# Optimization experiments

Measured on AMD Instinct MI355X. Metric: run time of the kernel, lower is better.

## Reference

```python
import jax, jax.numpy as jnp
import numpy as np

NUM_HEADS = 16
D_MODEL = 1024
D_K = D_MODEL // NUM_HEADS


def setup_inputs() -> dict:
    key = jax.random.key(0)
    ks = jax.random.split(key, 6)
    B, S = 4, 2048
    x = jax.random.normal(ks[0], (B, S, D_MODEL), dtype=jnp.float32)
    scale = 1.0 / np.sqrt(D_MODEL)
    W_q = jax.random.normal(ks[1], (D_MODEL, D_MODEL), dtype=jnp.float32) * scale
    W_k = jax.random.normal(ks[2], (D_MODEL, D_MODEL), dtype=jnp.float32) * scale
    W_v = jax.random.normal(ks[3], (D_MODEL, D_MODEL), dtype=jnp.float32) * scale
    W_o = jax.random.normal(ks[4], (D_MODEL, D_MODEL), dtype=jnp.float32) * scale
    b_o = jnp.zeros((D_MODEL,), dtype=jnp.float32)
    return {"x": x, "W_q": W_q, "W_k": W_k, "W_v": W_v, "W_o": W_o, "b_o": b_o}


def reference(x, W_q, W_k, W_v, W_o, b_o):
    B, S, D = x.shape
    H, dk = NUM_HEADS, D_K
    # torch nn.Linear computes x @ W.T
    q = (x @ W_q.T).reshape(B, S, H, dk).transpose(0, 2, 1, 3)  # [B,H,S,dk]
    k = (x @ W_k.T).reshape(B, S, H, dk).transpose(0, 2, 1, 3)
    v = (x @ W_v.T).reshape(B, S, H, dk).transpose(0, 2, 1, 3)
    scores = jnp.einsum('bhqd,bhkd->bhqk', q, k) / jnp.sqrt(jnp.float32(dk))
    causal = jnp.tril(jnp.ones((S, S), dtype=bool))  # allowed positions
    scores = jnp.where(causal[None, None], scores, -jnp.inf)
    attn = jax.nn.softmax(scores, axis=-1)
    out = jnp.einsum('bhqk,bhkd->bhqd', attn, v)
    combined = out.transpose(0, 2, 1, 3).reshape(B, S, D)
    return combined @ W_o.T + b_o
```

## Files before the change

kernel.cpp:

```cpp
#include <hip/hip_runtime.h>

typedef __attribute__((ext_vector_type(8))) short short8;
typedef __attribute__((ext_vector_type(4))) float f32x4;

#define GLOAD16(gp, lp)                                                        \
  __builtin_amdgcn_global_load_lds(                                            \
      (const __attribute__((address_space(1))) void*)(gp),                     \
      (__attribute__((address_space(3))) void*)(lp), 16, 0, 0)

__device__ __forceinline__ unsigned short f2bf(float f) {
  unsigned int u = __builtin_bit_cast(unsigned int, f);
  u += 0x7fffu + ((u >> 16) & 1u);
  return (unsigned short)(u >> 16);
}

__global__ __launch_bounds__(256) void cvt_f32_bf16(
    const float* __restrict__ src, unsigned short* __restrict__ dst, int n,
    float scale) {
  int i = (blockIdx.x * 256 + threadIdx.x) * 8;
  if (i + 8 <= n) {
    float4 a = *(const float4*)(src + i);
    float4 b = *(const float4*)(src + i + 4);
    short8 r;
    r[0] = (short)f2bf(a.x * scale); r[1] = (short)f2bf(a.y * scale);
    r[2] = (short)f2bf(a.z * scale); r[3] = (short)f2bf(a.w * scale);
    r[4] = (short)f2bf(b.x * scale); r[5] = (short)f2bf(b.y * scale);
    r[6] = (short)f2bf(b.z * scale); r[7] = (short)f2bf(b.w * scale);
    *(short8*)(dst + i) = r;
  }
}

template <int BN, int OUTF32>
__global__ __launch_bounds__(512) void gemm_nt2(
    const unsigned short* __restrict__ A, const unsigned short* __restrict__ B,
    void* __restrict__ Cout, const float* __restrict__ bias, int M, int N,
    int K, int nwg_y) {
  constexpr int NF = BN / 64;
  constexpr int WNSZ = BN / 4;
  __shared__ __align__(16) unsigned short As[2][256][64];
  __shared__ __align__(16) unsigned short Bs[2][BN][64];

  const int nwg = gridDim.x;
  const int id = blockIdx.x;
  const int sw = (id & 7) * (nwg >> 3) + (id >> 3);
  const int bx = sw / nwg_y, by = sw % nwg_y;
  const int row0 = bx * 256, col0 = by * BN;

  const int tid = threadIdx.x;
  const int wave = tid >> 6, lane = tid & 63;
  const int wm = wave >> 2, wn = wave & 3;
  const int l15 = lane & 15, l16 = lane >> 4;
  const int lrow = lane >> 3, lcol = (lane & 7) * 8;
  const int wv8 = wave * 8;

  f32x4 acc[8][NF];
#pragma unroll
  for (int m = 0; m < 8; ++m)
#pragma unroll
    for (int n = 0; n < NF; ++n) acc[m][n] = f32x4{0.f, 0.f, 0.f, 0.f};

  const int nt = K >> 6;

#define STAGE_TILE(buf, k0)                                                    \
  {                                                                            \
    _Pragma("unroll") for (int j = 0; j < 4; ++j) {                            \
      const unsigned short* gp =                                               \
          A + (size_t)(row0 + j * 64 + wv8 + lrow) * K + (k0) + lcol;          \
      GLOAD16(gp, &As[buf][j * 64 + wv8][0]);                                  \
    }                                                                          \
    _Pragma("unroll") for (int j = 0; j < NF; ++j) {                           \
      const unsigned short* gp =                                               \
          B + (size_t)(col0 + j * 64 + wv8 + lrow) * K + (k0) + lcol;          \
      GLOAD16(gp, &Bs[buf][j * 64 + wv8][0]);                                  \
    }                                                                          \
  }

  STAGE_TILE(0, 0)
  __syncthreads();

  for (int t = 0; t < nt; ++t) {
    const int cur = t & 1;
    if (t + 1 < nt) STAGE_TILE(cur ^ 1, (t + 1) << 6)

#pragma unroll
    for (int kk = 0; kk < 2; ++kk) {
      short8 a[8], b[NF];
#pragma unroll
      for (int m = 0; m < 8; ++m)
        a[m] = *(const short8*)&As[cur][wm * 128 + m * 16 + l15][kk * 32 + l16 * 8];
#pragma unroll
      for (int n = 0; n < NF; ++n)
        b[n] = *(const short8*)&Bs[cur][wn * WNSZ + n * 16 + l15][kk * 32 + l16 * 8];
#pragma unroll
      for (int m = 0; m < 8; ++m)
#pragma unroll
        for (int n = 0; n < NF; ++n)
          acc[m][n] =
              __builtin_amdgcn_mfma_f32_16x16x32_bf16(a[m], b[n], acc[m][n], 0, 0, 0);
    }
    __syncthreads();
  }

#pragma unroll
  for (int m = 0; m < 8; ++m) {
    const int row = row0 + wm * 128 + m * 16 + l16 * 4;
#pragma unroll
    for (int n = 0; n < NF; ++n) {
      const int col = col0 + wn * WNSZ + n * 16 + l15;
      float bv = 0.f;
      if (OUTF32) bv = bias[col];
#pragma unroll
      for (int r = 0; r < 4; ++r) {
        const float v = acc[m][n][r] + bv;
        if (OUTF32)
          ((float*)Cout)[(size_t)(row + r) * N + col] = v;
        else
          ((unsigned short*)Cout)[(size_t)(row + r) * N + col] = f2bf(v);
      }
    }
  }
#undef STAGE_TILE
}

__global__ __launch_bounds__(256) void attn_fwd(
    const unsigned short* __restrict__ QKV, unsigned short* __restrict__ AO) {
  const int S = 2048, LD = 3072;
  const int qt = gridDim.x - 1 - blockIdx.x;
  const int bh = blockIdx.y, b = bh >> 4, h = bh & 15;
  const int tid = threadIdx.x, wave = tid >> 6, lane = tid & 63;
  const int l15 = lane & 15, l16 = lane >> 4;
  const int q0 = qt * 64;

  __shared__ __align__(16) char KsB[2][64 * 128];
  __shared__ __align__(16) char VTB[2][64 * 128];
  __shared__ __align__(16) char PlB[4][16 * 128];

  const unsigned short* qptr =
      QKV + (size_t)(b * S + q0 + wave * 16 + l15) * LD + h * 64 + l16 * 8;
  short8 qf[2];
  qf[0] = *(const short8*)(qptr);
  qf[1] = *(const short8*)(qptr + 32);

  const int krow = lane >> 3;
  const int kcol = (((lane & 7) ^ (lane >> 3)) & 7) * 8;
  const int vp_ = tid & 31, vd0 = (tid >> 5) * 8;

  float mrow = -1e30f, lsum = 0.f;
  f32x4 accO[4] = {};
  const int nkv = qt + 1;

  {
#pragma unroll
    for (int i = 0; i < 2; ++i) {
      const int c = i * 4 + wave;
      const unsigned short* gp =
          QKV + (size_t)(b * S + c * 8 + krow) * LD + 1024 + h * 64 + kcol;
      GLOAD16(gp, KsB[0] + c * 1024);
    }
    const unsigned short* vp =
        QKV + (size_t)(b * S + 2 * vp_) * LD + 2048 + h * 64 + vd0;
    short8 va = *(const short8*)vp;
    short8 vb = *(const short8*)(vp + LD);
    uint4 vaw = __builtin_bit_cast(uint4, va);
    uint4 vbw = __builtin_bit_cast(uint4, vb);
    const unsigned int aw[4] = {vaw.x, vaw.y, vaw.z, vaw.w};
    const unsigned int bw[4] = {vbw.x, vbw.y, vbw.z, vbw.w};
#pragma unroll
    for (int w = 0; w < 4; ++w) {
      unsigned int e = __builtin_amdgcn_perm(bw[w], aw[w], 0x05040100u);
      unsigned int o = __builtin_amdgcn_perm(bw[w], aw[w], 0x07060302u);
      *(unsigned int*)(VTB[0] + (((vd0 + 2 * w) * 128 + 4 * vp_) ^ ((2 * w) << 4))) = e;
      *(unsigned int*)(VTB[0] + (((vd0 + 2 * w + 1) * 128 + 4 * vp_) ^ ((2 * w + 1) << 4))) = o;
    }
  }
  __syncthreads();

  for (int t = 0; t < nkv; ++t) {
    const int cur = t & 1, kv0 = t * 64;

    f32x4 accS[4] = {};
#pragma unroll
    for (int sub = 0; sub < 4; ++sub) {
      const int rw = sub * 16 + l15;
#pragma unroll
      for (int kk = 0; kk < 2; ++kk) {
        short8 kf = *(const short8*)(KsB[cur] + rw * 128 +
                                     ((kk * 64 + l16 * 16) ^ ((l15 & 7) << 4)));
        accS[sub] =
            __builtin_amdgcn_mfma_f32_16x16x32_bf16(kf, qf[kk], accS[sub], 0, 0, 0);
      }
    }

    short8 va, vb;
    const bool pre = (t + 1 < nkv);
    if (pre) {
      const int kvn = kv0 + 64;
#pragma unroll
      for (int i = 0; i < 2; ++i) {
        const int c = i * 4 + wave;
        const unsigned short* gp =
            QKV + (size_t)(b * S + kvn + c * 8 + krow) * LD + 1024 + h * 64 + kcol;
        GLOAD16(gp, KsB[cur ^ 1] + c * 1024);
      }
      const unsigned short* vp =
          QKV + (size_t)(b * S + kvn + 2 * vp_) * LD + 2048 + h * 64 + vd0;
      va = *(const short8*)vp;
      vb = *(const short8*)(vp + LD);
    }

    const bool nm = (kv0 + 63 > q0 + wave * 16);
    float mx = -1e30f;
    if (nm) {
      const int qabs = q0 + wave * 16 + l15;
#pragma unroll
      for (int sub = 0; sub < 4; ++sub)
#pragma unroll
        for (int r = 0; r < 4; ++r) {
          float s = accS[sub][r];
          if (kv0 + sub * 16 + l16 * 4 + r > qabs) s = -1e30f;
          accS[sub][r] = s;
          mx = fmaxf(mx, s);
        }
    } else {
#pragma unroll
      for (int sub = 0; sub < 4; ++sub)
#pragma unroll
        for (int r = 0; r < 4; ++r) mx = fmaxf(mx, accS[sub][r]);
    }
    mx = fmaxf(mx, __shfl_xor(mx, 16));
    mx = fmaxf(mx, __shfl_xor(mx, 32));

    if (__any(mx > mrow + 8.0f)) {
      const float mnew = fmaxf(mrow, mx);
      const float alpha = exp2f(mrow - mnew);
      mrow = mnew;
      lsum *= alpha;
      float al[4];
#pragma unroll
      for (int r = 0; r < 4; ++r) al[r] = __shfl(alpha, l16 * 4 + r);
#pragma unroll
      for (int sd = 0; sd < 4; ++sd)
#pragma unroll
        for (int r = 0; r < 4; ++r) accO[sd][r] *= al[r];
    }

    float rs = 0.f;
#pragma unroll
    for (int sub = 0; sub < 4; ++sub) {
      float p0 = exp2f(accS[sub][0] - mrow);
      float p1 = exp2f(accS[sub][1] - mrow);
      float p2 = exp2f(accS[sub][2] - mrow);
      float p3 = exp2f(accS[sub][3] - mrow);
      rs += (p0 + p1) + (p2 + p3);
      unsigned int pk01, pk23;
      asm("v_cvt_pk_bf16_f32 %0, %1, %2" : "=v"(pk01) : "v"(p0), "v"(p1));
      asm("v_cvt_pk_bf16_f32 %0, %1, %2" : "=v"(pk23) : "v"(p2), "v"(p3));
      uint2 pw = {pk01, pk23};
      *(uint2*)(PlB[wave] +
                ((l15 * 128 + sub * 32 + l16 * 8) ^ ((l15 & 7) << 4))) = pw;
    }
    rs += __shfl_xor(rs, 16);
    rs += __shfl_xor(rs, 32);
    lsum += rs;

    if (pre) {
      uint4 vaw = __builtin_bit_cast(uint4, va);
      uint4 vbw = __builtin_bit_cast(uint4, vb);
      const unsigned int aw[4] = {vaw.x, vaw.y, vaw.z, vaw.w};
      const unsigned int bw[4] = {vbw.x, vbw.y, vbw.z, vbw.w};
#pragma unroll
      for (int w = 0; w < 4; ++w) {
        unsigned int e = __builtin_amdgcn_perm(bw[w], aw[w], 0x05040100u);
        unsigned int o = __builtin_amdgcn_perm(bw[w], aw[w], 0x07060302u);
        *(unsigned int*)(VTB[cur ^ 1] +
                         (((vd0 + 2 * w) * 128 + 4 * vp_) ^ ((2 * w) << 4))) = e;
        *(unsigned int*)(VTB[cur ^ 1] +
                         (((vd0 + 2 * w + 1) * 128 + 4 * vp_) ^ ((2 * w + 1) << 4))) = o;
      }
    }

#pragma unroll
    for (int kk = 0; kk < 2; ++kk) {
      short8 pf = *(const short8*)(PlB[wave] + ((l15 * 128 + kk * 64 + l16 * 16) ^
                                               ((l15 & 7) << 4)));
#pragma unroll
      for (int sd = 0; sd < 4; ++sd) {
        short8 vf = *(const short8*)(VTB[cur] + (sd * 16 + l15) * 128 +
                                     ((kk * 64 + l16 * 16) ^ ((l15 & 7) << 4)));
        accO[sd] =
            __builtin_amdgcn_mfma_f32_16x16x32_bf16(pf, vf, accO[sd], 0, 0, 0);
      }
    }
    __syncthreads();
  }

  float ls[4];
#pragma unroll
  for (int r = 0; r < 4; ++r) ls[r] = __shfl(lsum, l16 * 4 + r);
#pragma unroll
  for (int sd = 0; sd < 4; ++sd)
#pragma unroll
    for (int r = 0; r < 4; ++r) {
      AO[(size_t)(b * S + q0 + wave * 16 + l16 * 4 + r) * 1024 + h * 64 +
         sd * 16 + l15] = f2bf(accO[sd][r] / ls[r]);
    }
}

extern "C" void kernel_launch(void* const* d_in, const int* in_sizes, int n_in,
                              void* d_out, int out_size, void* d_ws,
                              size_t ws_size, hipStream_t stream) {
  const float* x = (const float*)d_in[0];
  const float* Wq = (const float*)d_in[1];
  const float* Wk = (const float*)d_in[2];
  const float* Wv = (const float*)d_in[3];
  const float* Wo = (const float*)d_in[4];
  const float* bo = (const float*)d_in[5];

  char* ws = (char*)d_ws;
  unsigned short* xb = (unsigned short*)(ws);
  unsigned short* Wqkv = (unsigned short*)(ws + (size_t)(16 << 20));
  unsigned short* Wob = (unsigned short*)(ws + (size_t)(22 << 20));
  unsigned short* QKV = (unsigned short*)(ws + (size_t)(24 << 20));
  unsigned short* AO = (unsigned short*)(ws + (size_t)(72 << 20));

  const int M = 8192, D = 1024;
  const float QSCALE = 0.125f * 1.44269504088896340736f;

  cvt_f32_bf16<<<M * D / 2048, 256, 0, stream>>>(x, xb, M * D, 1.0f);
  cvt_f32_bf16<<<D * D / 2048, 256, 0, stream>>>(Wq, Wqkv, D * D, QSCALE);
  cvt_f32_bf16<<<D * D / 2048, 256, 0, stream>>>(Wk, Wqkv + D * D, D * D, 1.0f);
  cvt_f32_bf16<<<D * D / 2048, 256, 0, stream>>>(Wv, Wqkv + 2 * D * D, D * D, 1.0f);
  cvt_f32_bf16<<<D * D / 2048, 256, 0, stream>>>(Wo, Wob, D * D, 1.0f);

  gemm_nt2<256, 0><<<(M / 256) * (3072 / 256), 512, 0, stream>>>(
      xb, Wqkv, QKV, nullptr, M, 3072, D, 3072 / 256);

  dim3 g2(32, 64);
  attn_fwd<<<g2, 256, 0, stream>>>(QKV, AO);

  gemm_nt2<128, 1><<<(M / 256) * (D / 128), 512, 0, stream>>>(
      AO, Wob, d_out, bo, M, D, D, D / 128);
}
```

Baseline: 361.8 us.

## Enlarge attention query tile to 128, merge weight casts, retile QKV GEMM

The attention kernel now uses 512 threads, with 8 waves covering 128 query rows per block. Half of the waves issue the K loads and the other half load and transpose V, so each K/V tile staged in shared memory is reused by twice as many query rows. The four weight-conversion launches are merged into one 2D-grid kernel to cut launch overhead. The QKV GEMM N-tile changes from 256 to 192, which gives more workgroups (512 instead of 384) for better CU occupancy. The larger attention block raises register and LDS pressure per block and coarsens causal load balancing across blocks.

```diff
diff --git a/kernel.cpp b/kernel.cpp
--- a/kernel.cpp
+++ b/kernel.cpp
@@ -30,6 +30,28 @@
   }
 }
 
+__global__ __launch_bounds__(256) void cvt_w4(
+    const float* __restrict__ Wq, const float* __restrict__ Wk,
+    const float* __restrict__ Wv, const float* __restrict__ Wo,
+    unsigned short* __restrict__ Wqkv, unsigned short* __restrict__ Wob,
+    int DD, float qscale) {
+  const int y = blockIdx.y;
+  const float* src = (y == 0) ? Wq : (y == 1) ? Wk : (y == 2) ? Wv : Wo;
+  unsigned short* dst = (y < 3) ? Wqkv + (size_t)y * DD : Wob;
+  const float scale = (y == 0) ? qscale : 1.0f;
+  int i = (blockIdx.x * 256 + threadIdx.x) * 8;
+  if (i + 8 <= DD) {
+    float4 a = *(const float4*)(src + i);
+    float4 b = *(const float4*)(src + i + 4);
+    short8 r;
+    r[0] = (short)f2bf(a.x * scale); r[1] = (short)f2bf(a.y * scale);
+    r[2] = (short)f2bf(a.z * scale); r[3] = (short)f2bf(a.w * scale);
+    r[4] = (short)f2bf(b.x * scale); r[5] = (short)f2bf(b.y * scale);
+    r[6] = (short)f2bf(b.z * scale); r[7] = (short)f2bf(b.w * scale);
+    *(short8*)(dst + i) = r;
+  }
+}
+
 template <int BN, int OUTF32>
 __global__ __launch_bounds__(512) void gemm_nt2(
     const unsigned short* __restrict__ A, const unsigned short* __restrict__ B,
@@ -122,18 +144,18 @@
 #undef STAGE_TILE
 }
 
-__global__ __launch_bounds__(256) void attn_fwd(
+__global__ __launch_bounds__(512) void attn_fwd(
     const unsigned short* __restrict__ QKV, unsigned short* __restrict__ AO) {
   const int S = 2048, LD = 3072;
   const int qt = gridDim.x - 1 - blockIdx.x;
   const int bh = blockIdx.y, b = bh >> 4, h = bh & 15;
   const int tid = threadIdx.x, wave = tid >> 6, lane = tid & 63;
   const int l15 = lane & 15, l16 = lane >> 4;
-  const int q0 = qt * 64;
+  const int q0 = qt * 128;
 
   __shared__ __align__(16) char KsB[2][64 * 128];
   __shared__ __align__(16) char VTB[2][64 * 128];
-  __shared__ __align__(16) char PlB[4][16 * 128];
+  __shared__ __align__(16) char PlB[8][16 * 128];
 
   const unsigned short* qptr =
       QKV + (size_t)(b * S + q0 + wave * 16 + l15) * LD + h * 64 + l16 * 8;
@@ -143,34 +165,37 @@
 
   const int krow = lane >> 3;
   const int kcol = (((lane & 7) ^ (lane >> 3)) & 7) * 8;
-  const int vp_ = tid & 31, vd0 = (tid >> 5) * 8;
+  const int vp_ = tid & 31, vd0 = ((tid >> 5) & 7) * 8;
 
   float mrow = -1e30f, lsum = 0.f;
   f32x4 accO[4] = {};
-  const int nkv = qt + 1;
+  const int nkv = 2 * qt + 2;
 
   {
-#pragma unroll
-    for (int i = 0; i < 2; ++i) {
-      const int c = i * 4 + wave;
-      const unsigned short* gp =
-          QKV + (size_t)(b * S + c * 8 + krow) * LD + 1024 + h * 64 + kcol;
-      GLOAD16(gp, KsB[0] + c * 1024);
-    }
-    const unsigned short* vp =
-        QKV + (size_t)(b * S + 2 * vp_) * LD + 2048 + h * 64 + vd0;
-    short8 va = *(const short8*)vp;
-    short8 vb = *(const short8*)(vp + LD);
-    uint4 vaw = __builtin_bit_cast(uint4, va);
-    uint4 vbw = __builtin_bit_cast(uint4, vb);
-    const unsigned int aw[4] = {vaw.x, vaw.y, vaw.z, vaw.w};
-    const unsigned int bw[4] = {vbw.x, vbw.y, vbw.z, vbw.w};
-#pragma unroll
-    for (int w = 0; w < 4; ++w) {
-      unsigned int e = __builtin_amdgcn_perm(bw[w], aw[w], 0x05040100u);
-      unsigned int o = __builtin_amdgcn_perm(bw[w], aw[w], 0x07060302u);
-      *(unsigned int*)(VTB[0] + (((vd0 + 2 * w) * 128 + 4 * vp_) ^ ((2 * w) << 4))) = e;
-      *(unsigned int*)(VTB[0] + (((vd0 + 2 * w + 1) * 128 + 4 * vp_) ^ ((2 * w + 1) << 4))) = o;
+    if (wave >= 4) {
+#pragma unroll
+      for (int i = 0; i < 2; ++i) {
+        const int c = (wave - 4) * 2 + i;
+        const unsigned short* gp =
+            QKV + (size_t)(b * S + c * 8 + krow) * LD + 1024 + h * 64 + kcol;
+        GLOAD16(gp, KsB[0] + c * 1024);
+      }
+    } else {
+      const unsigned short* vp =
+          QKV + (size_t)(b * S + 2 * vp_) * LD + 2048 + h * 64 + vd0;
+      short8 va = *(const short8*)vp;
+      short8 vb = *(const short8*)(vp + LD);
+      uint4 vaw = __builtin_bit_cast(uint4, va);
+      uint4 vbw = __builtin_bit_cast(uint4, vb);
+      const unsigned int aw[4] = {vaw.x, vaw.y, vaw.z, vaw.w};
+      const unsigned int bw[4] = {vbw.x, vbw.y, vbw.z, vbw.w};
+#pragma unroll
+      for (int w = 0; w < 4; ++w) {
+        unsigned int e = __builtin_amdgcn_perm(bw[w], aw[w], 0x05040100u);
+        unsigned int o = __builtin_amdgcn_perm(bw[w], aw[w], 0x07060302u);
+        *(unsigned int*)(VTB[0] + (((vd0 + 2 * w) * 128 + 4 * vp_) ^ ((2 * w) << 4))) = e;
+        *(unsigned int*)(VTB[0] + (((vd0 + 2 * w + 1) * 128 + 4 * vp_) ^ ((2 * w + 1) << 4))) = o;
+      }
     }
   }
   __syncthreads();
@@ -195,17 +220,20 @@
     const bool pre = (t + 1 < nkv);
     if (pre) {
       const int kvn = kv0 + 64;
-#pragma unroll
-      for (int i = 0; i < 2; ++i) {
-        const int c = i * 4 + wave;
-        const unsigned short* gp =
-            QKV + (size_t)(b * S + kvn + c * 8 + krow) * LD + 1024 + h * 64 + kcol;
-        GLOAD16(gp, KsB[cur ^ 1] + c * 1024);
-      }
-      const unsigned short* vp =
-          QKV + (size_t)(b * S + kvn + 2 * vp_) * LD + 2048 + h * 64 + vd0;
-      va = *(const short8*)vp;
-      vb = *(const short8*)(vp + LD);
+      if (wave >= 4) {
+#pragma unroll
+        for (int i = 0; i < 2; ++i) {
+          const int c = (wave - 4) * 2 + i;
+          const unsigned short* gp =
+              QKV + (size_t)(b * S + kvn + c * 8 + krow) * LD + 1024 + h * 64 + kcol;
+          GLOAD16(gp, KsB[cur ^ 1] + c * 1024);
+        }
+      } else {
+        const unsigned short* vp =
+            QKV + (size_t)(b * S + kvn + 2 * vp_) * LD + 2048 + h * 64 + vd0;
+        va = *(const short8*)vp;
+        vb = *(const short8*)(vp + LD);
+      }
     }
 
     const bool nm = (kv0 + 63 > q0 + wave * 16);
@@ -263,7 +291,7 @@
     rs += __shfl_xor(rs, 32);
     lsum += rs;
 
-    if (pre) {
+    if (pre && wave < 4) {
       uint4 vaw = __builtin_bit_cast(uint4, va);
       uint4 vbw = __builtin_bit_cast(uint4, vb);
       const unsigned int aw[4] = {vaw.x, vaw.y, vaw.z, vaw.w};
@@ -327,16 +355,14 @@
   const float QSCALE = 0.125f * 1.44269504088896340736f;
 
   cvt_f32_bf16<<<M * D / 2048, 256, 0, stream>>>(x, xb, M * D, 1.0f);
-  cvt_f32_bf16<<<D * D / 2048, 256, 0, stream>>>(Wq, Wqkv, D * D, QSCALE);
-  cvt_f32_bf16<<<D * D / 2048, 256, 0, stream>>>(Wk, Wqkv + D * D, D * D, 1.0f);
-  cvt_f32_bf16<<<D * D / 2048, 256, 0, stream>>>(Wv, Wqkv + 2 * D * D, D * D, 1.0f);
-  cvt_f32_bf16<<<D * D / 2048, 256, 0, stream>>>(Wo, Wob, D * D, 1.0f);
-
-  gemm_nt2<256, 0><<<(M / 256) * (3072 / 256), 512, 0, stream>>>(
-      xb, Wqkv, QKV, nullptr, M, 3072, D, 3072 / 256);
-
-  dim3 g2(32, 64);
-  attn_fwd<<<g2, 256, 0, stream>>>(QKV, AO);
+  dim3 gw(D * D / 2048, 4);
+  cvt_w4<<<gw, 256, 0, stream>>>(Wq, Wk, Wv, Wo, Wqkv, Wob, D * D, QSCALE);
+
+  gemm_nt2<192, 0><<<(M / 256) * (3072 / 192), 512, 0, stream>>>(
+      xb, Wqkv, QKV, nullptr, M, 3072, D, 3072 / 192);
+
+  dim3 g2(16, 64);
+  attn_fwd<<<g2, 512, 0, stream>>>(QKV, AO);
 
   gemm_nt2<128, 1><<<(M / 256) * (D / 128), 512, 0, stream>>>(
       AO, Wob, d_out, bo, M, D, D, D / 128);
```

Measured after the change: 329.2 us. -9.0%, faster.
